# Performance work log

Measured on AMD Instinct MI355X. Metric: run time of the kernel, lower is better.

Reference implementation:

```python
import jax, jax.numpy as jnp
import numpy as np

N, T, D, H = 64, 1024, 512, 512

def setup_inputs() -> dict:
    key = jax.random.key(0)
    k1, k2, k3, k4 = jax.random.split(key, 4)
    x = jax.random.normal(k1, (N, T, D), dtype=jnp.float32)
    h0 = jax.random.normal(k2, (N, H), dtype=jnp.float32)
    Wx = jax.random.normal(k3, (D, H), dtype=jnp.float32) / jnp.sqrt(jnp.float32(D))
    Wh = jax.random.normal(k4, (H, H), dtype=jnp.float32) / jnp.sqrt(jnp.float32(H))
    b = jnp.zeros((H,), dtype=jnp.float32)
    return {"x": x, "h0": h0, "Wx": Wx, "Wh": Wh, "b": b}

def reference(x, h0, Wx, Wh, b):
    # Precompute input projection for all timesteps: (N,T,H)
    xW = jnp.einsum('ntd,dh->nth', x, Wx) + b
    # Sequential recurrence over time via lax.scan
    def step(prev_h, xw_t):
        next_h = jnp.tanh(prev_h @ Wh + xw_t)  # (N,H)
        return next_h, next_h
    # scan over time axis: move T to leading axis
    _, h_seq = jax.lax.scan(step, h0, jnp.swapaxes(xW, 0, 1))  # (T,N,H)
    return jnp.swapaxes(h_seq, 0, 1)  # (N,T,H)
```

## Files before the change

kernel.cpp:

```cpp
#include <hip/hip_runtime.h>
#include <hip/hip_fp16.h>
#include <cstddef>
#include <cstdint>

#define NB 64
#define TT 1024
#define DD 512
#define HH 512

typedef _Float16 h2_t __attribute__((ext_vector_type(2)));
typedef __attribute__((ext_vector_type(8))) short bf16x8;
typedef __attribute__((ext_vector_type(4))) float f32x4;
typedef __attribute__((ext_vector_type(8))) unsigned short ushort8;

__device__ __forceinline__ float dot2f(uint32_t a, uint32_t b, float c) {
#if __has_builtin(__builtin_amdgcn_fdot2)
    return __builtin_amdgcn_fdot2(__builtin_bit_cast(h2_t, a),
                                  __builtin_bit_cast(h2_t, b), c, false);
#else
    __half2 av = __builtin_bit_cast(__half2, a);
    __half2 bv = __builtin_bit_cast(__half2, b);
    float2 af = __half22float2(av), bf = __half22float2(bv);
    return fmaf(af.x, bf.x, fmaf(af.y, bf.y, c));
#endif
}

__device__ __forceinline__ float fast_tanh(float z) {
    z = fmaxf(-15.f, fminf(15.f, z));
    float u = __builtin_amdgcn_exp2f(-2.885390082f * z);
    return (1.f - u) * __builtin_amdgcn_rcpf(1.f + u);
}

__device__ __forceinline__ unsigned short f2bf(float f) {
    uint32_t u = __builtin_bit_cast(uint32_t, f);
    u += 0x7FFFu + ((u >> 16) & 1u);
    return (unsigned short)(u >> 16);
}

__global__ void conv_wt(const float* __restrict__ W,
                        unsigned short* __restrict__ Wt) {
    int n = blockIdx.x;
    int kc = threadIdx.x;
    ushort8 o;
#pragma unroll
    for (int i = 0; i < 8; ++i)
        o[i] = f2bf(W[(size_t)(kc * 8 + i) * HH + n]);
    *reinterpret_cast<ushort8*>(&Wt[(size_t)n * DD + kc * 8]) = o;
}

#define GBM 128
#define GBN 128
#define GBK 64
#define LDSW 72

__global__ __launch_bounds__(256, 4) void gemm_bf16f(
    const float* __restrict__ X,
    const unsigned short* __restrict__ Bt,
    const float* __restrict__ bias,
    float* __restrict__ C)
{
    __shared__ unsigned short As[GBM * LDSW];
    __shared__ unsigned short Bs[GBN * LDSW];

    const int tid  = threadIdx.x;
    const int m0   = blockIdx.x * GBM;
    const int n0   = blockIdx.y * GBN;
    const int lane = tid & 63;
    const int wave = tid >> 6;
    const int wm   = wave >> 1;
    const int wn   = wave & 1;

    const int axr = tid >> 1;
    const int axc = (tid & 1) * 32;
    const int srow = tid >> 3;
    const int sch  = tid & 7;

    f32x4 acc[4][4] = {};

    const int arow = wm * 64 + (lane & 15);
    const int brow = wn * 64 + (lane & 15);
    const int koff = (lane >> 4) * 8;

    for (int kt = 0; kt < DD / GBK; ++kt) {
        const int k0 = kt * GBK;
        {
            const float* xp = &X[(size_t)(m0 + axr) * DD + k0 + axc];
#pragma unroll
            for (int i = 0; i < 4; ++i) {
                float4 a = *reinterpret_cast<const float4*>(&xp[i * 8]);
                float4 b = *reinterpret_cast<const float4*>(&xp[i * 8 + 4]);
                ushort8 o;
                o[0] = f2bf(a.x); o[1] = f2bf(a.y);
                o[2] = f2bf(a.z); o[3] = f2bf(a.w);
                o[4] = f2bf(b.x); o[5] = f2bf(b.y);
                o[6] = f2bf(b.z); o[7] = f2bf(b.w);
                *reinterpret_cast<ushort8*>(&As[axr * LDSW + axc + i * 8]) = o;
            }
        }
#pragma unroll
        for (int p = 0; p < 4; ++p) {
            const int row = srow + p * 32;
            *reinterpret_cast<ushort8*>(&Bs[row * LDSW + sch * 8]) =
                *reinterpret_cast<const ushort8*>(
                    &Bt[(size_t)(n0 + row) * DD + k0 + sch * 8]);
        }
        __syncthreads();

#pragma unroll
        for (int kk = 0; kk < GBK; kk += 32) {
            bf16x8 af[4], bf[4];
#pragma unroll
            for (int mt = 0; mt < 4; ++mt)
                af[mt] = *reinterpret_cast<const bf16x8*>(
                    &As[(arow + mt * 16) * LDSW + kk + koff]);
#pragma unroll
            for (int nt = 0; nt < 4; ++nt)
                bf[nt] = *reinterpret_cast<const bf16x8*>(
                    &Bs[(brow + nt * 16) * LDSW + kk + koff]);
#pragma unroll
            for (int mt = 0; mt < 4; ++mt)
#pragma unroll
                for (int nt = 0; nt < 4; ++nt)
                    acc[mt][nt] = __builtin_amdgcn_mfma_f32_16x16x32_bf16(
                        af[mt], bf[nt], acc[mt][nt], 0, 0, 0);
        }
        __syncthreads();
    }

#pragma unroll
    for (int nt = 0; nt < 4; ++nt) {
        const int col = n0 + wn * 64 + nt * 16 + (lane & 15);
        const float bv = bias[col];
#pragma unroll
        for (int mt = 0; mt < 4; ++mt) {
            const int rbase = m0 + wm * 64 + mt * 16 + (lane >> 4) * 4;
#pragma unroll
            for (int r = 0; r < 4; ++r)
                C[(size_t)(rbase + r) * HH + col] = acc[mt][nt][r] + bv;
        }
    }
}

#define BM 128
#define BN 128
#define BK 8

__global__ __launch_bounds__(256, 2) void gemm_xw(
    const float* __restrict__ A,
    const float* __restrict__ B,
    const float* __restrict__ bias,
    float* __restrict__ C)
{
    __shared__ float As[BK][BM];
    __shared__ float Bs[BK][BN];

    const int tid  = threadIdx.x;
    const int tm   = tid >> 4;
    const int tn   = tid & 15;
    const int row0 = blockIdx.x * BM;
    const int col0 = blockIdx.y * BN;

    const int ar = tid >> 1;
    const int ac = (tid & 1) * 4;
    const int br = tid >> 5;
    const int bc = (tid & 31) * 4;

    float acc[8][8];
#pragma unroll
    for (int i = 0; i < 8; ++i)
#pragma unroll
        for (int j = 0; j < 8; ++j) acc[i][j] = 0.f;

    for (int k0 = 0; k0 < DD; k0 += BK) {
        float4 av = *reinterpret_cast<const float4*>(
            &A[(size_t)(row0 + ar) * DD + k0 + ac]);
        float4 bv = *reinterpret_cast<const float4*>(
            &B[(size_t)(k0 + br) * HH + col0 + bc]);

        As[ac + 0][ar] = av.x;
        As[ac + 1][ar] = av.y;
        As[ac + 2][ar] = av.z;
        As[ac + 3][ar] = av.w;
        *reinterpret_cast<float4*>(&Bs[br][bc]) = bv;
        __syncthreads();

#pragma unroll
        for (int kk = 0; kk < BK; ++kk) {
            float a[8], b[8];
            *reinterpret_cast<float4*>(&a[0]) =
                *reinterpret_cast<const float4*>(&As[kk][tm * 8]);
            *reinterpret_cast<float4*>(&a[4]) =
                *reinterpret_cast<const float4*>(&As[kk][tm * 8 + 4]);
            *reinterpret_cast<float4*>(&b[0]) =
                *reinterpret_cast<const float4*>(&Bs[kk][tn * 8]);
            *reinterpret_cast<float4*>(&b[4]) =
                *reinterpret_cast<const float4*>(&Bs[kk][tn * 8 + 4]);
#pragma unroll
            for (int i = 0; i < 8; ++i)
#pragma unroll
                for (int j = 0; j < 8; ++j)
                    acc[i][j] = fmaf(a[i], b[j], acc[i][j]);
        }
        __syncthreads();
    }

#pragma unroll
    for (int i = 0; i < 8; ++i) {
        const int row = row0 + tm * 8 + i;
#pragma unroll
        for (int j = 0; j < 8; j += 4) {
            const int col = col0 + tn * 8 + j;
            float4 o;
            o.x = acc[i][j + 0] + bias[col + 0];
            o.y = acc[i][j + 1] + bias[col + 1];
            o.z = acc[i][j + 2] + bias[col + 2];
            o.w = acc[i][j + 3] + bias[col + 3];
            *reinterpret_cast<float4*>(&C[(size_t)row * HH + col]) = o;
        }
    }
}

__global__ __launch_bounds__(1024, 4) void rnn_scan_l2a(
    const float* __restrict__ Wh,
    const float* __restrict__ h0,
    float* __restrict__ out,
    uint64_t* __restrict__ truth,
    uint64_t* __restrict__ mirror,
    int* __restrict__ meta)
{
    __shared__ __align__(16) uint32_t hp[2][HH / 2];
    __shared__ float partial[16][128];
    __shared__ int sh_batch, sh_role, sh_fast;

    const int tid = threadIdx.x;

    int xcd_raw;
    asm volatile("s_getreg_b32 %0, hwreg(HW_REG_XCC_ID)" : "=s"(xcd_raw));
    const int xcd = xcd_raw & 7;

    if (tid == 0) {
        int pos = __hip_atomic_fetch_add(&meta[xcd], 1, __ATOMIC_RELAXED,
                                         __HIP_MEMORY_SCOPE_AGENT);
        __hip_atomic_fetch_add(&meta[8], 1, __ATOMIC_RELEASE,
                               __HIP_MEMORY_SCOPE_AGENT);
        while (__hip_atomic_load(&meta[8], __ATOMIC_ACQUIRE,
                                 __HIP_MEMORY_SCOPE_AGENT) < 256)
            __builtin_amdgcn_s_sleep(8);
        int c[8];
#pragma unroll
        for (int q = 0; q < 8; ++q)
            c[q] = __hip_atomic_load(&meta[q], __ATOMIC_RELAXED,
                                     __HIP_MEMORY_SCOPE_AGENT);
        int totalfull = 0, basefull = 0, rembase = 0;
#pragma unroll
        for (int q = 0; q < 8; ++q) totalfull += c[q] >> 2;
        for (int q = 0; q < xcd; ++q) {
            basefull += c[q] >> 2;
            rembase  += c[q] & 3;
        }
        const int nf4 = (c[xcd] >> 2) << 2;
        if (pos < nf4) {
            sh_batch = basefull + (pos >> 2);
            sh_role  = pos & 3;
            sh_fast  = 1;
        } else {
            int ridx = rembase + (pos - nf4);
            sh_batch = totalfull + (ridx >> 2);
            sh_role  = ridx & 3;
            sh_fast  = 0;
        }
    }
    __syncthreads();

    const int n    = sh_batch;
    const int jb   = sh_role << 7;
    const int fast = sh_fast;

    const int w = tid >> 6;
    const int l = tid & 63;

    uint32_t w0[16], w1[16];
    {
        const float* wc = Wh + (size_t)(w * 32) * HH + jb + l;
#pragma unroll
        for (int p = 0; p < 16; ++p) {
            float e0 = wc[(size_t)(2 * p) * HH];
            float e1 = wc[(size_t)(2 * p + 1) * HH];
            w0[p] = __builtin_bit_cast(uint32_t, __floats2half2_rn(e0, e1));
            float f0 = wc[(size_t)(2 * p) * HH + 64];
            float f1 = wc[(size_t)(2 * p + 1) * HH + 64];
            w1[p] = __builtin_bit_cast(uint32_t, __floats2half2_rn(f0, f1));
        }
    }

    if (tid < HH)
        ((__half*)hp[0])[tid] = __float2half(h0[(size_t)n * HH + tid]);
    __syncthreads();

    float* outn = out + (size_t)n * TT * HH;
    uint64_t* tru = truth  + (size_t)n * 2 * HH;
    uint64_t* mir = mirror + (size_t)n * 2 * HH;

    const int rcol = (jb + 128 + (tid - 128)) & (HH - 1);

    int cur = 0;
    for (int t = 0; t < TT; ++t) {
        const uint32_t T = (uint32_t)(t + 1);
        const int slot = (int)(T & 1u);

        float xw_r = 0.f;
        if (tid < 128) xw_r = outn[(size_t)t * HH + jb + tid];

        const uint32_t* hpw = &hp[cur][w * 16];
        float a0 = 0.f, a1 = 0.f, b0 = 0.f, b1 = 0.f;
#pragma unroll
        for (int q = 0; q < 4; ++q) {
            uint4 hv = ((const uint4*)hpw)[q];
            a0 = dot2f(hv.x, w0[4 * q + 0], a0);
            b0 = dot2f(hv.x, w1[4 * q + 0], b0);
            a1 = dot2f(hv.y, w0[4 * q + 1], a1);
            b1 = dot2f(hv.y, w1[4 * q + 1], b1);
            a0 = dot2f(hv.z, w0[4 * q + 2], a0);
            b0 = dot2f(hv.z, w1[4 * q + 2], b0);
            a1 = dot2f(hv.w, w0[4 * q + 3], a1);
            b1 = dot2f(hv.w, w1[4 * q + 3], b1);
        }
        partial[w][l] = a0 + a1;
        partial[w][64 + l] = b0 + b1;
        __syncthreads();

        __half* hpn = (__half*)hp[cur ^ 1];
        if (tid < 128) {
            float s = 0.f;
#pragma unroll
            for (int ww = 0; ww < 16; ++ww) s += partial[ww][tid];
            float h = fast_tanh(s + xw_r);
            uint64_t pk = ((uint64_t)T << 32) |
                          (uint64_t)__builtin_bit_cast(uint32_t, h);
            const int off = slot * HH + jb + tid;
            if (fast) {
                asm volatile("global_atomic_swap_x2 %0, %1, off"
                             :: "v"((uint64_t)&mir[off]), "v"(pk) : "memory");
            }
            outn[(size_t)t * HH + jb + tid] = h;
            hpn[jb + tid] = __float2half(h);
            __hip_atomic_store(&tru[off], pk, __ATOMIC_RELAXED,
                               __HIP_MEMORY_SCOPE_AGENT);
        } else if (tid < 512) {
            const int off = slot * HH + rcol;
            uint64_t v;
            if (fast) {
                const uint64_t maddr = (uint64_t)&mir[off];
                const uint64_t zero = 0;
                int spins = 0;
                while (true) {
                    asm volatile(
                        "global_atomic_add_x2 %0, %1, %2, off sc0\n\t"
                        "s_waitcnt vmcnt(0)"
                        : "=v"(v) : "v"(maddr), "v"(zero) : "memory");
                    if ((uint32_t)(v >> 32) == T) break;
                    if ((++spins & 7) == 0) {
                        v = __hip_atomic_load(&tru[off], __ATOMIC_RELAXED,
                                              __HIP_MEMORY_SCOPE_AGENT);
                        if ((uint32_t)(v >> 32) == T) break;
                    }
                }
            } else {
                v = __hip_atomic_load(&tru[off], __ATOMIC_RELAXED,
                                      __HIP_MEMORY_SCOPE_AGENT);
                while ((uint32_t)(v >> 32) != T) {
                    __builtin_amdgcn_s_sleep(1);
                    v = __hip_atomic_load(&tru[off], __ATOMIC_RELAXED,
                                          __HIP_MEMORY_SCOPE_AGENT);
                }
            }
            hpn[rcol] = __float2half(__builtin_bit_cast(float, (uint32_t)v));
        }
        __syncthreads();
        cur ^= 1;
    }
}

__global__ __launch_bounds__(512, 2) void rnn_scan_f32(
    const float* __restrict__ Wh,
    const float* __restrict__ h0,
    float* __restrict__ out)
{
    __shared__ float hbuf[2][HH];
    const int n = blockIdx.x;
    const int j = threadIdx.x;

    hbuf[0][j] = h0[(size_t)n * HH + j];
    __syncthreads();

    float* outn = out + (size_t)n * TT * HH;
    const float* __restrict__ wp = Wh + j;

    int cur = 0;
    for (int t = 0; t < TT; ++t) {
        float acc = outn[(size_t)t * HH + j];
        const float* hc = hbuf[cur];
#pragma unroll 4
        for (int k = 0; k < HH; k += 4) {
            float4 hv = *reinterpret_cast<const float4*>(&hc[k]);
            acc = fmaf(hv.x, wp[(size_t)(k + 0) * HH], acc);
            acc = fmaf(hv.y, wp[(size_t)(k + 1) * HH], acc);
            acc = fmaf(hv.z, wp[(size_t)(k + 2) * HH], acc);
            acc = fmaf(hv.w, wp[(size_t)(k + 3) * HH], acc);
        }
        float hn = tanhf(acc);
        outn[(size_t)t * HH + j] = hn;
        hbuf[cur ^ 1][j] = hn;
        cur ^= 1;
        __syncthreads();
    }
}

extern "C" void kernel_launch(void* const* d_in, const int* in_sizes, int n_in,
                              void* d_out, int out_size, void* d_ws, size_t ws_size,
                              hipStream_t stream) {
    const float* x  = (const float*)d_in[0];
    const float* h0 = (const float*)d_in[1];
    const float* Wx = (const float*)d_in[2];
    const float* Wh = (const float*)d_in[3];
    const float* b  = (const float*)d_in[4];
    float* out = (float*)d_out;

    const long   M      = (long)NB * TT;
    const size_t pkt_b  = (size_t)NB * 2 * HH * 8;
    const size_t meta_b = 4096;
    const size_t wt_b   = (size_t)HH * DD * 2;

    const size_t off_mir  = pkt_b;
    const size_t off_meta = 2 * pkt_b;
    const size_t off_wt   = 2 * pkt_b + meta_b;
    const size_t need_all = off_wt + wt_b;
    const size_t need_mid = 2 * pkt_b + meta_b;

    if (ws_size >= need_all) {
        uint64_t*       truth  = (uint64_t*)d_ws;
        uint64_t*       mirror = (uint64_t*)((char*)d_ws + off_mir);
        int*            meta   = (int*)((char*)d_ws + off_meta);
        unsigned short* Wt     = (unsigned short*)((char*)d_ws + off_wt);

        conv_wt<<<HH, 64, 0, stream>>>(Wx, Wt);
        dim3 gg(M / GBM, HH / GBN);
        gemm_bf16f<<<gg, 256, 0, stream>>>(x, Wt, b, out);
        hipMemsetAsync(meta, 0, 64, stream);
        rnn_scan_l2a<<<256, 1024, 0, stream>>>(Wh, h0, out, truth, mirror, meta);
    } else if (ws_size >= need_mid) {
        uint64_t* truth  = (uint64_t*)d_ws;
        uint64_t* mirror = (uint64_t*)((char*)d_ws + off_mir);
        int*      meta   = (int*)((char*)d_ws + off_meta);
        dim3 g1(M / BM, HH / BN);
        gemm_xw<<<g1, 256, 0, stream>>>(x, Wx, b, out);
        hipMemsetAsync(meta, 0, 64, stream);
        rnn_scan_l2a<<<256, 1024, 0, stream>>>(Wh, h0, out, truth, mirror, meta);
    } else {
        dim3 g1(M / BM, HH / BN);
        gemm_xw<<<g1, 256, 0, stream>>>(x, Wx, b, out);
        rnn_scan_f32<<<NB, 512, 0, stream>>>(Wh, h0, out);
    }
}
```

Before: 1.640 ms.

## Pack two fp16 hidden values per exchange packet in RNN scan

Each cross-block exchange packet now carries two fp16 hidden values plus the step tag instead of one fp32 value, halving the number of packets written and polled per step. Only 64 threads produce and 192 threads poll per block, the fast path writes only the mirror and not the truth buffer, and the polling loop drops the periodic truth fallback in favour of a short sleep. This cuts atomic traffic and spinning on the critical path of the sequential recurrence. In exchange, remote hidden values arrive already rounded to fp16, and the fast path now depends entirely on the mirror atomics for progress.

```diff
diff --git a/kernel.cpp b/kernel.cpp
--- a/kernel.cpp
+++ b/kernel.cpp
@@ -220,7 +220,7 @@
     }
 }
 
-__global__ __launch_bounds__(1024, 4) void rnn_scan_l2a(
+__global__ __launch_bounds__(1024, 4) void rnn_scan_pk2(
     const float* __restrict__ Wh,
     const float* __restrict__ h0,
     float* __restrict__ out,
@@ -274,6 +274,7 @@
 
     const int n    = sh_batch;
     const int jb   = sh_role << 7;
+    const int pb   = sh_role << 6;
     const int fast = sh_fast;
 
     const int w = tid >> 6;
@@ -298,18 +299,20 @@
     __syncthreads();
 
     float* outn = out + (size_t)n * TT * HH;
-    uint64_t* tru = truth  + (size_t)n * 2 * HH;
-    uint64_t* mir = mirror + (size_t)n * 2 * HH;
-
-    const int rcol = (jb + 128 + (tid - 128)) & (HH - 1);
+    uint64_t* tru = truth  + (size_t)n * 2 * 256;
+    uint64_t* mir = mirror + (size_t)n * 2 * 256;
+
+    const int ppi = (pb + 64 + (tid - 64)) & 255;
 
     int cur = 0;
     for (int t = 0; t < TT; ++t) {
         const uint32_t T = (uint32_t)(t + 1);
         const int slot = (int)(T & 1u);
 
-        float xw_r = 0.f;
-        if (tid < 128) xw_r = outn[(size_t)t * HH + jb + tid];
+        float2 xw2 = {0.f, 0.f};
+        if (tid < 64)
+            xw2 = *reinterpret_cast<const float2*>(
+                &outn[(size_t)t * HH + jb + 2 * tid]);
 
         const uint32_t* hpw = &hp[cur][w * 16];
         float a0 = 0.f, a1 = 0.f, b0 = 0.f, b1 = 0.f;
@@ -329,52 +332,56 @@
         partial[w][64 + l] = b0 + b1;
         __syncthreads();
 
-        __half* hpn = (__half*)hp[cur ^ 1];
-        if (tid < 128) {
-            float s = 0.f;
-#pragma unroll
-            for (int ww = 0; ww < 16; ++ww) s += partial[ww][tid];
-            float h = fast_tanh(s + xw_r);
-            uint64_t pk = ((uint64_t)T << 32) |
-                          (uint64_t)__builtin_bit_cast(uint32_t, h);
-            const int off = slot * HH + jb + tid;
+        uint32_t* hpn32 = hp[cur ^ 1];
+        if (tid < 64) {
+            float s0 = 0.f, s1 = 0.f;
+#pragma unroll
+            for (int ww = 0; ww < 16; ++ww) {
+                float2 pv = *reinterpret_cast<const float2*>(
+                    &partial[ww][2 * tid]);
+                s0 += pv.x; s1 += pv.y;
+            }
+            float hh0 = fast_tanh(s0 + xw2.x);
+            float hh1 = fast_tanh(s1 + xw2.y);
+            uint32_t ph = __builtin_bit_cast(uint32_t,
+                                             __floats2half2_rn(hh0, hh1));
+            uint64_t pk = ((uint64_t)T << 32) | ph;
+            const int idx = slot * 256 + pb + tid;
             if (fast) {
                 asm volatile("global_atomic_swap_x2 %0, %1, off"
-                             :: "v"((uint64_t)&mir[off]), "v"(pk) : "memory");
+                             :: "v"((uint64_t)&mir[idx]), "v"(pk) : "memory");
+            } else {
+                __hip_atomic_store(&tru[idx], pk, __ATOMIC_RELAXED,
+                                   __HIP_MEMORY_SCOPE_AGENT);
             }
-            outn[(size_t)t * HH + jb + tid] = h;
-            hpn[jb + tid] = __float2half(h);
-            __hip_atomic_store(&tru[off], pk, __ATOMIC_RELAXED,
-                               __HIP_MEMORY_SCOPE_AGENT);
-        } else if (tid < 512) {
-            const int off = slot * HH + rcol;
+            float2 ov; ov.x = hh0; ov.y = hh1;
+            *reinterpret_cast<float2*>(
+                &outn[(size_t)t * HH + jb + 2 * tid]) = ov;
+            hpn32[pb + tid] = ph;
+        } else if (tid < 256) {
+            const int idx = slot * 256 + ppi;
             uint64_t v;
             if (fast) {
-                const uint64_t maddr = (uint64_t)&mir[off];
+                const uint64_t maddr = (uint64_t)&mir[idx];
                 const uint64_t zero = 0;
-                int spins = 0;
                 while (true) {
                     asm volatile(
                         "global_atomic_add_x2 %0, %1, %2, off sc0\n\t"
                         "s_waitcnt vmcnt(0)"
                         : "=v"(v) : "v"(maddr), "v"(zero) : "memory");
                     if ((uint32_t)(v >> 32) == T) break;
-                    if ((++spins & 7) == 0) {
-                        v = __hip_atomic_load(&tru[off], __ATOMIC_RELAXED,
-                                              __HIP_MEMORY_SCOPE_AGENT);
-                        if ((uint32_t)(v >> 32) == T) break;
-                    }
+                    __builtin_amdgcn_s_sleep(1);
                 }
             } else {
-                v = __hip_atomic_load(&tru[off], __ATOMIC_RELAXED,
+                v = __hip_atomic_load(&tru[idx], __ATOMIC_RELAXED,
                                       __HIP_MEMORY_SCOPE_AGENT);
                 while ((uint32_t)(v >> 32) != T) {
                     __builtin_amdgcn_s_sleep(1);
-                    v = __hip_atomic_load(&tru[off], __ATOMIC_RELAXED,
+                    v = __hip_atomic_load(&tru[idx], __ATOMIC_RELAXED,
                                           __HIP_MEMORY_SCOPE_AGENT);
                 }
             }
-            hpn[rcol] = __float2half(__builtin_bit_cast(float, (uint32_t)v));
+            hpn32[ppi] = (uint32_t)v;
         }
         __syncthreads();
         cur ^= 1;
@@ -427,7 +434,7 @@
     float* out = (float*)d_out;
 
     const long   M      = (long)NB * TT;
-    const size_t pkt_b  = (size_t)NB * 2 * HH * 8;
+    const size_t pkt_b  = (size_t)NB * 2 * 256 * 8;
     const size_t meta_b = 4096;
     const size_t wt_b   = (size_t)HH * DD * 2;
 
@@ -447,7 +454,7 @@
         dim3 gg(M / GBM, HH / GBN);
         gemm_bf16f<<<gg, 256, 0, stream>>>(x, Wt, b, out);
         hipMemsetAsync(meta, 0, 64, stream);
-        rnn_scan_l2a<<<256, 1024, 0, stream>>>(Wh, h0, out, truth, mirror, meta);
+        rnn_scan_pk2<<<256, 1024, 0, stream>>>(Wh, h0, out, truth, mirror, meta);
     } else if (ws_size >= need_mid) {
         uint64_t* truth  = (uint64_t*)d_ws;
         uint64_t* mirror = (uint64_t*)((char*)d_ws + off_mir);
@@ -455,7 +462,7 @@
         dim3 g1(M / BM, HH / BN);
         gemm_xw<<<g1, 256, 0, stream>>>(x, Wx, b, out);
         hipMemsetAsync(meta, 0, 64, stream);
-        rnn_scan_l2a<<<256, 1024, 0, stream>>>(Wh, h0, out, truth, mirror, meta);
+        rnn_scan_pk2<<<256, 1024, 0, stream>>>(Wh, h0, out, truth, mirror, meta);
     } else {
         dim3 g1(M / BM, HH / BN);
         gemm_xw<<<g1, 256, 0, stream>>>(x, Wx, b, out);
```

Result: faster. 1.542 ms (-5.9%).
